# Optimization experiments

Hardware: AMD Instinct MI355X
Metric: run time of the kernel (lower is better)

Reference implementation:

```python
import jax, jax.numpy as jnp
import numpy as np

B, L, E, H = 512, 32, 2048, 32
D = E // H  # 64


def setup_inputs() -> dict:
    key = jax.random.key(0)
    ks = jax.random.split(key, 10)
    s = 0.02
    return {
        "x": jax.random.normal(ks[0], (B, L, E), dtype=jnp.float32),
        "wq": jax.random.normal(ks[1], (E, E), dtype=jnp.float32) * s,
        "bq": jnp.zeros((E,), dtype=jnp.float32),
        "wk": jax.random.normal(ks[2], (E, E), dtype=jnp.float32) * s,
        "bk": jnp.zeros((E,), dtype=jnp.float32),
        "wv": jax.random.normal(ks[3], (E, E), dtype=jnp.float32) * s,
        "bv": jnp.zeros((E,), dtype=jnp.float32),
        "wo": jax.random.normal(ks[4], (E, E), dtype=jnp.float32) * s,
        "bo": jnp.zeros((E,), dtype=jnp.float32),
        "rel_pos_enc": jax.random.normal(ks[5], (2 * 32 - 1, D), dtype=jnp.float32),
    }


def reference(x, wq, bq, wk, bk, wv, bv, wo, bo, rel_pos_enc):
    b, l, e = x.shape
    h, d = H, D
    scale = d ** -0.5
    # projections (torch Linear: x @ W.T + b)
    q = (x @ wq.T + bq).reshape(b, l, h, d).transpose(0, 2, 1, 3)  # [B,H,L,D]
    k = (x @ wk.T + bk).reshape(b, l, h, d).transpose(0, 2, 1, 3)
    v = (x @ wv.T + bv).reshape(b, l, h, d).transpose(0, 2, 1, 3)
    scores = jnp.einsum("bhid,bhjd->bhij", q, k) * scale  # [B,H,L,L]
    # relative position gather: idx[i,j] = i - j + (L-1) in [0, 2L-2]
    pos = jnp.arange(l)
    rel_idx = pos[:, None] - pos[None, :] + (l - 1)
    rel_pos = rel_pos_enc[rel_idx]  # [L,L,D]
    # faithful to torch broadcasted matmul (batch dims (B,H) vs (L,), H==L):
    # rel_score[b,h,i,j] = sum_d q[b,h,i,d] * rel_pos[h,j,d]
    scores = scores + jnp.einsum("bhid,hjd->bhij", q, rel_pos)
    attn = jax.nn.softmax(scores, axis=-1)  # dropout p=0 (eval)
    out = jnp.einsum("bhij,bhjd->bhid", attn, v)  # [B,H,L,D]
    out = out.transpose(0, 2, 1, 3).reshape(b, l, e)
    return out @ wo.T + bo
```

## Files before the change

kernel.cpp:

```cpp
#include <hip/hip_runtime.h>
#include <hip/hip_bf16.h>
#include <stdint.h>

typedef __bf16 bf16x8 __attribute__((ext_vector_type(8)));
typedef float f32x4 __attribute__((ext_vector_type(4)));
typedef unsigned short u16x8 __attribute__((ext_vector_type(8)));
typedef unsigned short u16x4 __attribute__((ext_vector_type(4)));

#define G_AS __attribute__((address_space(1)))
#define L_AS __attribute__((address_space(3)))

__device__ __forceinline__ void gload_lds16(const void* g, void* l) {
  __builtin_amdgcn_global_load_lds((G_AS void*)g, (L_AS void*)l, 16, 0, 0);
}

__device__ __forceinline__ float b2f(unsigned short u) {
  union { float f; unsigned int i; } cv;
  cv.i = ((unsigned int)u) << 16;
  return cv.f;
}

__device__ __forceinline__ unsigned short f2b(float f) {
  unsigned int u = __float_as_uint(f);
  unsigned int r = u + 0x7FFFu + ((u >> 16) & 1u);
  return (unsigned short)(r >> 16);
}


__global__ void k_cast_f32_bf16(const float* __restrict__ src,
                                unsigned short* __restrict__ dst, int n4) {
  int i = blockIdx.x * blockDim.x + threadIdx.x;
  if (i >= n4) return;
  float4 v = reinterpret_cast<const float4*>(src)[i];
  u16x4 o;
  o[0] = f2b(v.x); o[1] = f2b(v.y); o[2] = f2b(v.z); o[3] = f2b(v.w);
  reinterpret_cast<u16x4*>(dst)[i] = o;
}

__global__ void k_build_wqkv(const float* __restrict__ wq, const float* __restrict__ wk,
                             const float* __restrict__ wv, unsigned short* __restrict__ dst) {
  int i = blockIdx.x * blockDim.x + threadIdx.x;
  if (i >= 3145728) return;
  int e = i << 2;
  int row = e >> 11;
  int col = e & 2047;
  const float* src; float sc = 1.0f;
  if (row < 2048) { src = wq + ((size_t)row << 11); }
  else if (row < 4096) { src = wk + ((size_t)(row - 2048) << 11); sc = 0.125f; }
  else { src = wv + ((size_t)(row - 4096) << 11); }
  float4 v = *reinterpret_cast<const float4*>(src + col);
  u16x4 o;
  o[0] = f2b(v.x * sc); o[1] = f2b(v.y * sc); o[2] = f2b(v.z * sc); o[3] = f2b(v.w * sc);
  *reinterpret_cast<u16x4*>(dst + e) = o;
}

__global__ void k_build_bqkv(const float* __restrict__ bq, const float* __restrict__ bk,
                             const float* __restrict__ bv, float* __restrict__ dst) {
  int i = blockIdx.x * blockDim.x + threadIdx.x;
  if (i >= 6144) return;
  float v;
  if (i < 2048) v = bq[i];
  else if (i < 4096) v = bk[i - 2048] * 0.125f;
  else v = bv[i - 4096];
  dst[i] = v;
}

__global__ void k_build_rel(const float* __restrict__ rpe, unsigned short* __restrict__ dst) {
  int i = blockIdx.x * blockDim.x + threadIdx.x;
  if (i >= 16384) return;
  int h = i >> 9;
  int j = (i >> 4) & 31;
  int d = (i & 15) << 2;
  const float* s = rpe + (size_t)(h - j + 31) * 64 + d;
  float4 v = *reinterpret_cast<const float4*>(s);
  u16x4 o;
  o[0] = f2b(v.x); o[1] = f2b(v.y); o[2] = f2b(v.z); o[3] = f2b(v.w);
  *reinterpret_cast<u16x4*>(dst + ((size_t)i << 2)) = o;
}


template <int OUT_F32>
__global__ __launch_bounds__(512, 2)
void k_gemm256(const unsigned short* __restrict__ A,
               const unsigned short* __restrict__ B,
               const float* __restrict__ bias,
               void* __restrict__ Cptr,
               int M, int N, int K)
{
  __shared__ __align__(16) unsigned short As[3][8192];
  __shared__ __align__(16) unsigned short Bs[3][8192];

  const int nbn = N >> 8;
  const int cpx = gridDim.x >> 3;
  const int orig = blockIdx.x;
  const int wg = (orig & 7) * cpx + (orig >> 3);
  const int bm = wg / nbn;
  const int bn = wg % nbn;

  const int tid = threadIdx.x;
  const int lane = tid & 63;
  const int wid = tid >> 6;
  const int wr = wid >> 2;
  const int wc = wid & 3;

  const int rs = tid >> 2;
  const int cs = ((tid & 3) ^ ((tid >> 3) & 3)) << 3;
  const unsigned short* agA0 = A + (size_t)(bm * 256 + rs) * K + cs;
  const unsigned short* agA1 = agA0 + (size_t)128 * K;
  const unsigned short* agB0 = B + (size_t)(bn * 256 + rs) * K + cs;
  const unsigned short* agB1 = agB0 + (size_t)128 * K;
  const int ldst = tid * 8;

  const int fr = lane & 15;
  const int q  = lane >> 4;
  const int sx = q ^ ((fr >> 1) & 3);
  const int rbase = fr * 32 + sx * 8;
  const int aOff = wr * 4096 + rbase;
  const int bOff = wc * 2048 + rbase;

  f32x4 acc[8][4] = {};
  const int NT = K >> 5;

#pragma unroll
  for (int pf = 0; pf < 2; ++pf) {
    const int kof = pf << 5;
    gload_lds16(agA0 + kof, &As[pf][ldst]);
    gload_lds16(agA1 + kof, &As[pf][ldst + 4096]);
    gload_lds16(agB0 + kof, &Bs[pf][ldst]);
    gload_lds16(agB1 + kof, &Bs[pf][ldst + 4096]);
  }
  asm volatile("s_waitcnt vmcnt(4)" ::: "memory");
  asm volatile("s_barrier" ::: "memory");

  int rb = 0;
  int sb = 2;
  for (int t = 0; t < NT; ++t) {
    const unsigned short* ab = &As[rb][0];
    const unsigned short* bb = &Bs[rb][0];
    const bool st = (t + 2) < NT;
    const int kof = (t + 2) << 5;

    bf16x8 afL[4], bf[4];
#pragma unroll
    for (int n = 0; n < 4; ++n)
      bf[n] = *reinterpret_cast<const bf16x8*>(bb + bOff + n * 512);
#pragma unroll
    for (int m = 0; m < 4; ++m)
      afL[m] = *reinterpret_cast<const bf16x8*>(ab + aOff + m * 512);
    if (st) {
      gload_lds16(agA0 + kof, &As[sb][ldst]);
      gload_lds16(agA1 + kof, &As[sb][ldst + 4096]);
    }
    __builtin_amdgcn_sched_barrier(0);
    asm volatile("s_barrier" ::: "memory");
    __builtin_amdgcn_sched_barrier(0);
    __builtin_amdgcn_s_setprio(1);
#pragma unroll
    for (int m = 0; m < 4; ++m)
#pragma unroll
      for (int n = 0; n < 4; ++n)
        acc[m][n] = __builtin_amdgcn_mfma_f32_16x16x32_bf16(afL[m], bf[n], acc[m][n], 0, 0, 0);
    __builtin_amdgcn_s_setprio(0);
    __builtin_amdgcn_sched_barrier(0);
    asm volatile("s_barrier" ::: "memory");

    bf16x8 afH[4];
#pragma unroll
    for (int m = 0; m < 4; ++m)
      afH[m] = *reinterpret_cast<const bf16x8*>(ab + aOff + (4 + m) * 512);
    if (st) {
      gload_lds16(agB0 + kof, &Bs[sb][ldst]);
      gload_lds16(agB1 + kof, &Bs[sb][ldst + 4096]);
    }
    if (t < NT - 2)       asm volatile("s_waitcnt vmcnt(4)" ::: "memory");
    else if (t == NT - 2) asm volatile("s_waitcnt vmcnt(0)" ::: "memory");
    __builtin_amdgcn_sched_barrier(0);
    asm volatile("s_barrier" ::: "memory");
    __builtin_amdgcn_sched_barrier(0);
    __builtin_amdgcn_s_setprio(1);
#pragma unroll
    for (int m = 0; m < 4; ++m)
#pragma unroll
      for (int n = 0; n < 4; ++n)
        acc[4 + m][n] = __builtin_amdgcn_mfma_f32_16x16x32_bf16(afH[m], bf[n], acc[4 + m][n], 0, 0, 0);
    __builtin_amdgcn_s_setprio(0);
    __builtin_amdgcn_sched_barrier(0);
    asm volatile("s_barrier" ::: "memory");

    rb = (rb == 2) ? 0 : rb + 1;
    sb = (sb == 2) ? 0 : sb + 1;
  }

  const int rBase = bm * 256 + wr * 128 + (q << 2);
  const int cBase = bn * 256 + wc * 64 + fr;
#pragma unroll
  for (int n = 0; n < 4; ++n) {
    const int col = cBase + n * 16;
    const float bv = bias[col];
#pragma unroll
    for (int m = 0; m < 8; ++m) {
      const int row = rBase + m * 16;
#pragma unroll
      for (int r = 0; r < 4; ++r) {
        float v = acc[m][n][r] + bv;
        if (OUT_F32) {
          reinterpret_cast<float*>(Cptr)[(size_t)(row + r) * N + col] = v;
        } else {
          reinterpret_cast<unsigned short*>(Cptr)[(size_t)(row + r) * N + col] = f2b(v);
        }
      }
    }
  }
}


__global__ __launch_bounds__(256)
void k_attn(const unsigned short* __restrict__ qkv,
            const unsigned short* __restrict__ relb,
            unsigned short* __restrict__ ctx)
{
  __shared__ float qL[32][68];
  __shared__ float krL[32][68];
  __shared__ float vL[32][68];
  __shared__ float SL[32][33];

  const int bh = blockIdx.x;
  const int b = bh >> 5;
  const int h = bh & 31;
  const int t = threadIdx.x;
  const int r = t >> 3;
  const int d0 = (t & 7) << 3;

  const unsigned short* base = qkv + (size_t)(b * 32 + r) * 6144 + h * 64 + d0;
  u16x8 uq = *reinterpret_cast<const u16x8*>(base);
  u16x8 uk = *reinterpret_cast<const u16x8*>(base + 2048);
  u16x8 uv = *reinterpret_cast<const u16x8*>(base + 4096);
  u16x8 ur = *reinterpret_cast<const u16x8*>(relb + (((size_t)(h * 32 + r)) << 6) + d0);

  float fq[8], fkr[8], fv[8];
#pragma unroll
  for (int c = 0; c < 8; ++c) {
    fq[c] = b2f(uq[c]);
    fkr[c] = b2f(uk[c]) + b2f(ur[c]);
    fv[c] = b2f(uv[c]);
  }
  *reinterpret_cast<float4*>(&qL[r][d0])      = make_float4(fq[0], fq[1], fq[2], fq[3]);
  *reinterpret_cast<float4*>(&qL[r][d0 + 4])  = make_float4(fq[4], fq[5], fq[6], fq[7]);
  *reinterpret_cast<float4*>(&krL[r][d0])     = make_float4(fkr[0], fkr[1], fkr[2], fkr[3]);
  *reinterpret_cast<float4*>(&krL[r][d0 + 4]) = make_float4(fkr[4], fkr[5], fkr[6], fkr[7]);
  *reinterpret_cast<float4*>(&vL[r][d0])      = make_float4(fv[0], fv[1], fv[2], fv[3]);
  *reinterpret_cast<float4*>(&vL[r][d0 + 4])  = make_float4(fv[4], fv[5], fv[6], fv[7]);
  __syncthreads();

  const int i = r;
  const int j0 = (t & 7) << 2;
  float s0 = 0.f, s1 = 0.f, s2 = 0.f, s3 = 0.f;
#pragma unroll
  for (int d = 0; d < 64; d += 4) {
    float4 qv = *reinterpret_cast<const float4*>(&qL[i][d]);
    float4 k0 = *reinterpret_cast<const float4*>(&krL[j0 + 0][d]);
    float4 k1 = *reinterpret_cast<const float4*>(&krL[j0 + 1][d]);
    float4 k2 = *reinterpret_cast<const float4*>(&krL[j0 + 2][d]);
    float4 k3 = *reinterpret_cast<const float4*>(&krL[j0 + 3][d]);
    s0 += qv.x * k0.x + qv.y * k0.y + qv.z * k0.z + qv.w * k0.w;
    s1 += qv.x * k1.x + qv.y * k1.y + qv.z * k1.z + qv.w * k1.w;
    s2 += qv.x * k2.x + qv.y * k2.y + qv.z * k2.z + qv.w * k2.w;
    s3 += qv.x * k3.x + qv.y * k3.y + qv.z * k3.z + qv.w * k3.w;
  }
  SL[i][j0 + 0] = s0; SL[i][j0 + 1] = s1; SL[i][j0 + 2] = s2; SL[i][j0 + 3] = s3;
  __syncthreads();

  float m = SL[i][0];
#pragma unroll
  for (int jj = 1; jj < 32; ++jj) m = fmaxf(m, SL[i][jj]);
  __syncthreads();

  float p0 = __expf(s0 - m), p1 = __expf(s1 - m), p2 = __expf(s2 - m), p3 = __expf(s3 - m);
  SL[i][j0 + 0] = p0; SL[i][j0 + 1] = p1; SL[i][j0 + 2] = p2; SL[i][j0 + 3] = p3;
  __syncthreads();

  float den = 0.f;
#pragma unroll
  for (int jj = 0; jj < 32; ++jj) den += SL[i][jj];
  const float inv = 1.0f / den;

  float o[8] = {0.f, 0.f, 0.f, 0.f, 0.f, 0.f, 0.f, 0.f};
#pragma unroll
  for (int jj = 0; jj < 32; ++jj) {
    float pj = SL[i][jj];
    float4 v0 = *reinterpret_cast<const float4*>(&vL[jj][d0]);
    float4 v1 = *reinterpret_cast<const float4*>(&vL[jj][d0 + 4]);
    o[0] += pj * v0.x; o[1] += pj * v0.y; o[2] += pj * v0.z; o[3] += pj * v0.w;
    o[4] += pj * v1.x; o[5] += pj * v1.y; o[6] += pj * v1.z; o[7] += pj * v1.w;
  }
  u16x8 ov;
#pragma unroll
  for (int c = 0; c < 8; ++c) ov[c] = f2b(o[c] * inv);
  *reinterpret_cast<u16x8*>(ctx + (size_t)(b * 32 + i) * 2048 + h * 64 + d0) = ov;
}


extern "C" void kernel_launch(void* const* d_in, const int* in_sizes, int n_in,
                              void* d_out, int out_size, void* d_ws, size_t ws_size,
                              hipStream_t stream) {
  const float* x   = (const float*)d_in[0];
  const float* wq  = (const float*)d_in[1];
  const float* bq  = (const float*)d_in[2];
  const float* wk  = (const float*)d_in[3];
  const float* bk  = (const float*)d_in[4];
  const float* wv  = (const float*)d_in[5];
  const float* bv  = (const float*)d_in[6];
  const float* wo  = (const float*)d_in[7];
  const float* bo  = (const float*)d_in[8];
  const float* rpe = (const float*)d_in[9];

  char* ws = (char*)d_ws;
  unsigned short* xb    = (unsigned short*)(ws);
  unsigned short* wqkvb = (unsigned short*)(ws + 67108864);
  unsigned short* wob   = (unsigned short*)(ws + 67108864 + 25165824);
  unsigned short* qkvb  = (unsigned short*)(ws + 67108864 + 25165824 + 8388608);
  float*          bqkv  = (float*)(ws + 67108864 + 25165824 + 8388608 + 201326592);
  unsigned short* relb  = (unsigned short*)(ws + 67108864 + 25165824 + 8388608 + 201326592 + 24576);

  k_cast_f32_bf16<<<32768, 256, 0, stream>>>(x, xb, 8388608);
  k_build_wqkv<<<12288, 256, 0, stream>>>(wq, wk, wv, wqkvb);
  k_cast_f32_bf16<<<4096, 256, 0, stream>>>(wo, wob, 1048576);
  k_build_bqkv<<<24, 256, 0, stream>>>(bq, bk, bv, bqkv);
  k_build_rel<<<64, 256, 0, stream>>>(rpe, relb);

  k_gemm256<0><<<(16384 / 256) * (6144 / 256), 512, 0, stream>>>(
      xb, wqkvb, bqkv, qkvb, 16384, 6144, 2048);

  k_attn<<<16384, 256, 0, stream>>>(qkvb, relb, xb);

  k_gemm256<1><<<(16384 / 256) * (2048 / 256), 512, 0, stream>>>(
      xb, wob, bo, (float*)d_out, 16384, 2048, 2048);
}
```

Measured before the change: 786.8 us.

## Deepen GEMM LDS pipeline to four stages and use shuffle-based softmax in attention

The GEMM kernel moves from a 3-stage to a 4-stage LDS ring buffer with three tiles prefetched, adjusting the vmcnt waits to match. LDS use grows to 128KB, so launch bounds drop to one block per CU. The attention kernel replaces the LDS-based row max and sum reductions, and their extra barriers, with wave shuffles, and writes already-normalized probabilities. It also changes LDS padding from 68 to 66 floats, which risks misaligned float4 LDS reads and bank conflicts.

```diff
diff --git a/kernel.cpp b/kernel.cpp
--- a/kernel.cpp
+++ b/kernel.cpp
@@ -80,15 +80,15 @@
 
 
 template <int OUT_F32>
-__global__ __launch_bounds__(512, 2)
+__global__ __launch_bounds__(512, 1)
 void k_gemm256(const unsigned short* __restrict__ A,
                const unsigned short* __restrict__ B,
                const float* __restrict__ bias,
                void* __restrict__ Cptr,
                int M, int N, int K)
 {
-  __shared__ __align__(16) unsigned short As[3][8192];
-  __shared__ __align__(16) unsigned short Bs[3][8192];
+  __shared__ __align__(16) unsigned short As[4][8192];
+  __shared__ __align__(16) unsigned short Bs[4][8192];
 
   const int nbn = N >> 8;
   const int cpx = gridDim.x >> 3;
@@ -122,23 +122,23 @@
   const int NT = K >> 5;
 
 #pragma unroll
-  for (int pf = 0; pf < 2; ++pf) {
+  for (int pf = 0; pf < 3; ++pf) {
     const int kof = pf << 5;
     gload_lds16(agA0 + kof, &As[pf][ldst]);
     gload_lds16(agA1 + kof, &As[pf][ldst + 4096]);
     gload_lds16(agB0 + kof, &Bs[pf][ldst]);
     gload_lds16(agB1 + kof, &Bs[pf][ldst + 4096]);
   }
-  asm volatile("s_waitcnt vmcnt(4)" ::: "memory");
+  asm volatile("s_waitcnt vmcnt(8)" ::: "memory");
   asm volatile("s_barrier" ::: "memory");
 
-  int rb = 0;
-  int sb = 2;
   for (int t = 0; t < NT; ++t) {
+    const int rb = t & 3;
+    const int sb = (t + 3) & 3;
     const unsigned short* ab = &As[rb][0];
     const unsigned short* bb = &Bs[rb][0];
-    const bool st = (t + 2) < NT;
-    const int kof = (t + 2) << 5;
+    const bool st = (t + 3) < NT;
+    const int kof = (t + 3) << 5;
 
     bf16x8 afL[4], bf[4];
 #pragma unroll
@@ -172,8 +172,9 @@
       gload_lds16(agB0 + kof, &Bs[sb][ldst]);
       gload_lds16(agB1 + kof, &Bs[sb][ldst + 4096]);
     }
-    if (t < NT - 2)       asm volatile("s_waitcnt vmcnt(4)" ::: "memory");
-    else if (t == NT - 2) asm volatile("s_waitcnt vmcnt(0)" ::: "memory");
+    if (st)                  asm volatile("s_waitcnt vmcnt(8)" ::: "memory");
+    else if (t + 2 < NT)     asm volatile("s_waitcnt vmcnt(4)" ::: "memory");
+    else if (t + 1 < NT)     asm volatile("s_waitcnt vmcnt(0)" ::: "memory");
     __builtin_amdgcn_sched_barrier(0);
     asm volatile("s_barrier" ::: "memory");
     __builtin_amdgcn_sched_barrier(0);
@@ -186,9 +187,6 @@
     __builtin_amdgcn_s_setprio(0);
     __builtin_amdgcn_sched_barrier(0);
     asm volatile("s_barrier" ::: "memory");
-
-    rb = (rb == 2) ? 0 : rb + 1;
-    sb = (sb == 2) ? 0 : sb + 1;
   }
 
   const int rBase = bm * 256 + wr * 128 + (q << 2);
@@ -219,10 +217,10 @@
             const unsigned short* __restrict__ relb,
             unsigned short* __restrict__ ctx)
 {
-  __shared__ float qL[32][68];
-  __shared__ float krL[32][68];
-  __shared__ float vL[32][68];
-  __shared__ float SL[32][33];
+  __shared__ float qL[32][66];
+  __shared__ float krL[32][66];
+  __shared__ float vL[32][66];
+  __shared__ float PL[32][33];
 
   const int bh = blockIdx.x;
   const int b = bh >> 5;
@@ -267,27 +265,25 @@
     s2 += qv.x * k2.x + qv.y * k2.y + qv.z * k2.z + qv.w * k2.w;
     s3 += qv.x * k3.x + qv.y * k3.y + qv.z * k3.z + qv.w * k3.w;
   }
-  SL[i][j0 + 0] = s0; SL[i][j0 + 1] = s1; SL[i][j0 + 2] = s2; SL[i][j0 + 3] = s3;
+
+  float mx = fmaxf(fmaxf(s0, s1), fmaxf(s2, s3));
+  mx = fmaxf(mx, __shfl_xor(mx, 1));
+  mx = fmaxf(mx, __shfl_xor(mx, 2));
+  mx = fmaxf(mx, __shfl_xor(mx, 4));
+  float p0 = __expf(s0 - mx), p1 = __expf(s1 - mx), p2 = __expf(s2 - mx), p3 = __expf(s3 - mx);
+  float sm = p0 + p1 + p2 + p3;
+  sm += __shfl_xor(sm, 1);
+  sm += __shfl_xor(sm, 2);
+  sm += __shfl_xor(sm, 4);
+  const float inv = 1.0f / sm;
+  PL[i][j0 + 0] = p0 * inv; PL[i][j0 + 1] = p1 * inv;
+  PL[i][j0 + 2] = p2 * inv; PL[i][j0 + 3] = p3 * inv;
   __syncthreads();
 
-  float m = SL[i][0];
-#pragma unroll
-  for (int jj = 1; jj < 32; ++jj) m = fmaxf(m, SL[i][jj]);
-  __syncthreads();
-
-  float p0 = __expf(s0 - m), p1 = __expf(s1 - m), p2 = __expf(s2 - m), p3 = __expf(s3 - m);
-  SL[i][j0 + 0] = p0; SL[i][j0 + 1] = p1; SL[i][j0 + 2] = p2; SL[i][j0 + 3] = p3;
-  __syncthreads();
-
-  float den = 0.f;
-#pragma unroll
-  for (int jj = 0; jj < 32; ++jj) den += SL[i][jj];
-  const float inv = 1.0f / den;
-
   float o[8] = {0.f, 0.f, 0.f, 0.f, 0.f, 0.f, 0.f, 0.f};
 #pragma unroll
   for (int jj = 0; jj < 32; ++jj) {
-    float pj = SL[i][jj];
+    float pj = PL[i][jj];
     float4 v0 = *reinterpret_cast<const float4*>(&vL[jj][d0]);
     float4 v1 = *reinterpret_cast<const float4*>(&vL[jj][d0 + 4]);
     o[0] += pj * v0.x; o[1] += pj * v0.y; o[2] += pj * v0.z; o[3] += pj * v0.w;
@@ -295,7 +291,7 @@
   }
   u16x8 ov;
 #pragma unroll
-  for (int c = 0; c < 8; ++c) ov[c] = f2b(o[c] * inv);
+  for (int c = 0; c < 8; ++c) ov[c] = f2b(o[c]);
   *reinterpret_cast<u16x8*>(ctx + (size_t)(b * 32 + i) * 2048 + h * 64 + d0) = ov;
 }
 
```

After: 833.7 us. +6.0%, slower.
